# Performance work log

Measured on AMD Instinct MI355X. Metric: run time of the kernel, lower is better.

The kernel has to match this reference:

```python
import jax, jax.numpy as jnp
import numpy as np

D_MODEL, D_K, D_V, H = 1024, 64, 64, 16


def setup_inputs() -> dict:
    key = jax.random.key(0)
    ks = jax.random.split(key, 11)
    b, nq, nk = 2, 2048, 2048
    queries = jax.random.normal(ks[0], (b, nq, D_MODEL), dtype=jnp.float32)
    keys = jax.random.normal(ks[1], (b, nk, D_MODEL), dtype=jnp.float32)
    values = jax.random.normal(ks[2], (b, nk, D_MODEL), dtype=jnp.float32)
    def xavier(k, shape):
        fan_in, fan_out = shape[1], shape[0]
        lim = np.sqrt(6.0 / (fan_in + fan_out)).astype(np.float32)
        return jax.random.uniform(k, shape, jnp.float32, -lim, lim)
    # torch Linear weight shape: (out_features, in_features)
    Wq = xavier(ks[3], (H * D_K, D_MODEL)); bq = jnp.zeros((H * D_K,), jnp.float32)
    Wk = xavier(ks[4], (H * D_K, D_MODEL)); bk = jnp.zeros((H * D_K,), jnp.float32)
    Wv = xavier(ks[5], (H * D_V, D_MODEL)); bv = jnp.zeros((H * D_V,), jnp.float32)
    Wo = xavier(ks[6], (D_MODEL, H * D_V)); bo = jnp.zeros((D_MODEL,), jnp.float32)
    return {"queries": queries, "keys": keys, "values": values,
            "Wq": Wq, "bq": bq, "Wk": Wk, "bk": bk,
            "Wv": Wv, "bv": bv, "Wo": Wo, "bo": bo}


def reference(queries, keys, values, Wq, bq, Wk, bk, Wv, bv, Wo, bo):
    b, nq, _ = queries.shape
    nk = keys.shape[1]
    scale = 1.0 / np.sqrt(D_K).astype(np.float32)
    # projections -> (b, h, n, d)
    q = (queries @ Wq.T + bq).reshape(b, nq, H, D_K).transpose(0, 2, 1, 3)
    k = (keys @ Wk.T + bk).reshape(b, nk, H, D_K).transpose(0, 2, 1, 3)
    v = (values @ Wv.T + bv).reshape(b, nk, H, D_V).transpose(0, 2, 1, 3)
    att = jnp.einsum('bhqd,bhkd->bhqk', q, k) * scale  # (b,h,nq,nk)
    att = jax.nn.softmax(att, axis=-1)
    out = jnp.einsum('bhqk,bhkd->bhqd', att, v)        # (b,h,nq,dv)
    out = out.transpose(0, 2, 1, 3).reshape(b, nq, H * D_V)
    return out @ Wo.T + bo
```

## Files before the change

kernel.cpp:

```cpp
#include <hip/hip_runtime.h>
#include <stdint.h>

typedef __bf16 v8bf __attribute__((ext_vector_type(8)));
typedef float  v4f  __attribute__((ext_vector_type(4)));

#define QSCALE 0.18033688011112042f

typedef __attribute__((address_space(3))) void lds_vp;
typedef const __attribute__((address_space(1))) void gbl_vp;
__device__ __forceinline__ void gl_lds16(const __bf16* g, __bf16* l) {
    __builtin_amdgcn_global_load_lds((gbl_vp*)g, (lds_vp*)l, 16, 0, 0);
}

__device__ __forceinline__ v8bf cvt8(const float* __restrict__ p) {
    float4 x = *reinterpret_cast<const float4*>(p);
    float4 y = *reinterpret_cast<const float4*>(p + 4);
    v8bf r;
    r[0] = (__bf16)x.x; r[1] = (__bf16)x.y; r[2] = (__bf16)x.z; r[3] = (__bf16)x.w;
    r[4] = (__bf16)y.x; r[5] = (__bf16)y.y; r[6] = (__bf16)y.z; r[7] = (__bf16)y.w;
    return r;
}

__global__ __launch_bounds__(256) void cvt_w(
    const float* __restrict__ w0, const float* __restrict__ w1,
    const float* __restrict__ w2, const float* __restrict__ w3,
    __bf16* __restrict__ o0, __bf16* __restrict__ o1,
    __bf16* __restrict__ o2, __bf16* __restrict__ o3)
{
    const float* src; __bf16* dst;
    switch (blockIdx.y) {
        case 0: src = w0; dst = o0; break;
        case 1: src = w1; dst = o1; break;
        case 2: src = w2; dst = o2; break;
        default: src = w3; dst = o3; break;
    }
    size_t i = ((size_t)blockIdx.x * 256 + threadIdx.x) * 8;
    *reinterpret_cast<v8bf*>(dst + i) = cvt8(src + i);
}

__global__ __launch_bounds__(256) void cvt_in(
    const float* __restrict__ i0, const float* __restrict__ i1,
    const float* __restrict__ i2,
    __bf16* __restrict__ o0, __bf16* __restrict__ o1, __bf16* __restrict__ o2)
{
    const float* src; __bf16* dst;
    switch (blockIdx.y) {
        case 0: src = i0; dst = o0; break;
        case 1: src = i1; dst = o1; break;
        default: src = i2; dst = o2; break;
    }
    size_t i = ((size_t)blockIdx.x * 256 + threadIdx.x) * 8;
    *reinterpret_cast<v8bf*>(dst + i) = cvt8(src + i);
}

template<int MT>
__device__ __forceinline__ void gemm_body(
    const __bf16* __restrict__ A, const __bf16* __restrict__ W,
    const float* __restrict__ bias, void* __restrict__ outp,
    int mode, float oscale, int bx, int by)
{
    constexpr int K = 1024, N = 1024;
    constexpr int WM = MT / 32;
    constexpr int AI = MT / 32;
    constexpr int BI = 4;
    __shared__ __align__(16) __bf16 As[MT * 64];
    __shared__ __align__(16) __bf16 Bs[128 * 64];

    const int lane = threadIdx.x & 63;
    const int wave = threadIdx.x >> 6;
    const int quad = lane >> 4;
    const int l15  = lane & 15;
    const int m_base = bx * MT;
    const int n_base = by * 128;
    const int wm = (wave & 1) * (MT / 2);
    const int wn = (wave >> 1) * 64;

    int arow[AI], acol[AI], brow[BI], bcol[BI];
    #pragma unroll
    for (int i = 0; i < AI; ++i) {
        int L = (i * 4 + wave) * 64 + lane;
        int r = L >> 3, s = L & 7;
        arow[i] = r; acol[i] = (s ^ (r & 7)) * 8;
    }
    #pragma unroll
    for (int i = 0; i < BI; ++i) {
        int L = (i * 4 + wave) * 64 + lane;
        int r = L >> 3, s = L & 7;
        brow[i] = r; bcol[i] = (s ^ (r & 7)) * 8;
    }

    v4f acc[WM][4];
    #pragma unroll
    for (int fa = 0; fa < WM; ++fa)
        #pragma unroll
        for (int fb = 0; fb < 4; ++fb) { v4f z = {0.f,0.f,0.f,0.f}; acc[fa][fb] = z; }

    for (int kb = 0; kb < K; kb += 64) {
        #pragma unroll
        for (int i = 0; i < AI; ++i)
            gl_lds16(A + (size_t)(m_base + arow[i]) * K + kb + acol[i],
                     &As[(size_t)(i * 4 + wave) * 512]);
        #pragma unroll
        for (int i = 0; i < BI; ++i)
            gl_lds16(W + (size_t)(n_base + brow[i]) * K + kb + bcol[i],
                     &Bs[(size_t)(i * 4 + wave) * 512]);
        __syncthreads();
        #pragma unroll
        for (int ks = 0; ks < 2; ++ks) {
            v8bf af[WM], bf[4];
            #pragma unroll
            for (int f = 0; f < WM; ++f) {
                const int R = wm + f * 16 + l15;
                const int slot = (ks * 4 + quad) ^ (R & 7);
                af[f] = *reinterpret_cast<const v8bf*>(&As[R * 64 + slot * 8]);
            }
            #pragma unroll
            for (int f = 0; f < 4; ++f) {
                const int R = wn + f * 16 + l15;
                const int slot = (ks * 4 + quad) ^ (R & 7);
                bf[f] = *reinterpret_cast<const v8bf*>(&Bs[R * 64 + slot * 8]);
            }
            #pragma unroll
            for (int fa = 0; fa < WM; ++fa)
                #pragma unroll
                for (int fb = 0; fb < 4; ++fb)
                    acc[fa][fb] = __builtin_amdgcn_mfma_f32_16x16x32_bf16(
                        af[fa], bf[fb], acc[fa][fb], 0, 0, 0);
        }
        __syncthreads();
    }

    #pragma unroll
    for (int fa = 0; fa < WM; ++fa)
        #pragma unroll
        for (int fb = 0; fb < 4; ++fb) {
            const int nc = n_base + wn + fb * 16 + l15;
            const float bval = bias[nc];
            #pragma unroll
            for (int r = 0; r < 4; ++r) {
                const int m = m_base + wm + fa * 16 + quad * 4 + r;
                const float v = (acc[fa][fb][r] + bval) * oscale;
                if (mode == 2) {
                    ((float*)outp)[(size_t)m * N + nc] = v;
                } else {
                    int b = m >> 11, n = m & 2047, h = nc >> 6, d = nc & 63;
                    size_t off = (mode == 0)
                        ? ((size_t)(b * 16 + h) * 2048 + n) * 64 + d
                        : ((size_t)(b * 16 + h) * 64 + d) * 2048 + n;
                    ((__bf16*)outp)[off] = (__bf16)v;
                }
            }
        }
}

__global__ __launch_bounds__(256) void qkv_gemm(
    const __bf16* __restrict__ Aq, const __bf16* __restrict__ Ak,
    const __bf16* __restrict__ Av,
    const __bf16* __restrict__ Wq, const __bf16* __restrict__ Wk,
    const __bf16* __restrict__ Wv,
    const float* __restrict__ bq, const float* __restrict__ bk,
    const float* __restrict__ bv,
    __bf16* __restrict__ Qo, __bf16* __restrict__ Ko, __bf16* __restrict__ Vo)
{
    const int id = blockIdx.x;
    const int by = id & 7;
    const int bx = (id >> 3) & 31;
    const int z  = id >> 8;

    const __bf16 *A, *W; const float* bias; __bf16* outp; float oscale; int mode;
    switch (z) {
        case 0:  A = Aq; W = Wq; bias = bq; outp = Qo; oscale = QSCALE; mode = 0; break;
        case 1:  A = Ak; W = Wk; bias = bk; outp = Ko; oscale = 1.0f;   mode = 0; break;
        default: A = Av; W = Wv; bias = bv; outp = Vo; oscale = 1.0f;   mode = 1; break;
    }
    gemm_body<128>(A, W, bias, outp, mode, oscale, bx, by);
}

__global__ __launch_bounds__(256) void out_gemm(
    const __bf16* __restrict__ A, const __bf16* __restrict__ W,
    const float* __restrict__ bias, float* __restrict__ outp)
{
    const int by = blockIdx.x & 7;
    const int bx = blockIdx.x >> 3;
    gemm_body<64>(A, W, bias, outp, 2, 1.0f, bx, by);
}

__global__ __launch_bounds__(256) void attn_kernel(
    const __bf16* __restrict__ Q, const __bf16* __restrict__ Kb_,
    const __bf16* __restrict__ Vt, __bf16* __restrict__ O)
{
    __shared__ __align__(16) __bf16 Ks[64 * 64];
    __shared__ __align__(16) __bf16 Vs[64 * 64];
    __shared__ __align__(16) __bf16 p_lds[4][16][72];

    const int lane = threadIdx.x & 63;
    const int wave = threadIdx.x >> 6;
    const int quad = lane >> 4;
    const int l15  = lane & 15;
    const int bh = blockIdx.x & 31;
    const int qt = blockIdx.x >> 5;
    const int b  = bh >> 4, h = bh & 15;

    const __bf16* Qh = Q   + (size_t)bh * 2048 * 64;
    const __bf16* Kh = Kb_ + (size_t)bh * 2048 * 64;
    const __bf16* Vh = Vt  + (size_t)bh * 64 * 2048;

    int srow[2], scol[2];
    #pragma unroll
    for (int i = 0; i < 2; ++i) {
        int L = (i * 4 + wave) * 64 + lane;
        int r = L >> 3, s = L & 7;
        srow[i] = r; scol[i] = (s ^ (r & 7)) * 8;
    }

    v8bf qf[2];
    #pragma unroll
    for (int ks = 0; ks < 2; ++ks)
        qf[ks] = *reinterpret_cast<const v8bf*>(
            Qh + (size_t)(qt * 64 + wave * 16 + l15) * 64 + ks * 32 + quad * 8);

    v4f o_acc[4];
    #pragma unroll
    for (int c = 0; c < 4; ++c) { v4f z = {0.f,0.f,0.f,0.f}; o_acc[c] = z; }
    float l_r[4];
    #pragma unroll
    for (int r = 0; r < 4; ++r) l_r[r] = 0.f;

    for (int kt = 0; kt < 32; ++kt) {
        #pragma unroll
        for (int i = 0; i < 2; ++i) {
            gl_lds16(Kh + (size_t)(kt * 64 + srow[i]) * 64 + scol[i],
                     &Ks[(size_t)(i * 4 + wave) * 512]);
            gl_lds16(Vh + (size_t)srow[i] * 2048 + kt * 64 + scol[i],
                     &Vs[(size_t)(i * 4 + wave) * 512]);
        }
        __syncthreads();

        v4f s_t[4];
        #pragma unroll
        for (int c = 0; c < 4; ++c) { v4f z = {0.f,0.f,0.f,0.f}; s_t[c] = z; }
        #pragma unroll
        for (int ks = 0; ks < 2; ++ks) {
            v8bf kf[4];
            #pragma unroll
            for (int c = 0; c < 4; ++c) {
                const int R = c * 16 + l15;
                const int slot = (ks * 4 + quad) ^ (R & 7);
                kf[c] = *reinterpret_cast<const v8bf*>(&Ks[R * 64 + slot * 8]);
            }
            #pragma unroll
            for (int c = 0; c < 4; ++c)
                s_t[c] = __builtin_amdgcn_mfma_f32_16x16x32_bf16(qf[ks], kf[c], s_t[c], 0, 0, 0);
        }

        #pragma unroll
        for (int r = 0; r < 4; ++r) {
            const float p0 = __builtin_exp2f(s_t[0][r]);
            const float p1 = __builtin_exp2f(s_t[1][r]);
            const float p2 = __builtin_exp2f(s_t[2][r]);
            const float p3 = __builtin_exp2f(s_t[3][r]);
            l_r[r] += (p0 + p1) + (p2 + p3);
            p_lds[wave][quad * 4 + r][0 * 16 + l15] = (__bf16)p0;
            p_lds[wave][quad * 4 + r][1 * 16 + l15] = (__bf16)p1;
            p_lds[wave][quad * 4 + r][2 * 16 + l15] = (__bf16)p2;
            p_lds[wave][quad * 4 + r][3 * 16 + l15] = (__bf16)p3;
        }

        #pragma unroll
        for (int ks = 0; ks < 2; ++ks) {
            v8bf vf[4];
            #pragma unroll
            for (int c = 0; c < 4; ++c) {
                const int R = c * 16 + l15;
                const int slot = (ks * 4 + quad) ^ (R & 7);
                vf[c] = *reinterpret_cast<const v8bf*>(&Vs[R * 64 + slot * 8]);
            }
            v8bf pf = *reinterpret_cast<const v8bf*>(&p_lds[wave][l15][ks * 32 + quad * 8]);
            #pragma unroll
            for (int c = 0; c < 4; ++c)
                o_acc[c] = __builtin_amdgcn_mfma_f32_16x16x32_bf16(pf, vf[c], o_acc[c], 0, 0, 0);
        }
        __syncthreads();
    }

    #pragma unroll
    for (int r = 0; r < 4; ++r) {
        float l = l_r[r];
        #pragma unroll
        for (int off = 1; off < 16; off <<= 1)
            l += __shfl_xor(l, off, 16);
        const float inv_l = 1.0f / l;
        const int qr = qt * 64 + wave * 16 + quad * 4 + r;
        #pragma unroll
        for (int c = 0; c < 4; ++c) {
            const int col = h * 64 + c * 16 + l15;
            O[(size_t)(b * 2048 + qr) * 1024 + col] = (__bf16)(o_acc[c][r] * inv_l);
        }
    }
}

extern "C" void kernel_launch(void* const* d_in, const int* in_sizes, int n_in,
                              void* d_out, int out_size, void* d_ws, size_t ws_size,
                              hipStream_t stream) {
    const float* q_in = (const float*)d_in[0];
    const float* k_in = (const float*)d_in[1];
    const float* v_in = (const float*)d_in[2];
    const float* Wq = (const float*)d_in[3];
    const float* bq = (const float*)d_in[4];
    const float* Wk = (const float*)d_in[5];
    const float* bk = (const float*)d_in[6];
    const float* Wv = (const float*)d_in[7];
    const float* bv = (const float*)d_in[8];
    const float* Wo = (const float*)d_in[9];
    const float* bo = (const float*)d_in[10];
    float* out = (float*)d_out;

    __bf16* ws  = (__bf16*)d_ws;
    __bf16* Abq = ws;
    __bf16* Abk = Abq + 4194304;
    __bf16* Abv = Abk + 4194304;
    __bf16* Qb  = Abv + 4194304;
    __bf16* Kb  = Qb  + 4194304;
    __bf16* Vb  = Kb  + 4194304;
    __bf16* Wqb = Vb  + 4194304;
    __bf16* Wkb = Wqb + 1048576;
    __bf16* Wvb = Wkb + 1048576;
    __bf16* Wob = Wvb + 1048576;
    __bf16* Ob  = Abq;

    cvt_w<<<dim3(512, 4), 256, 0, stream>>>(Wq, Wk, Wv, Wo, Wqb, Wkb, Wvb, Wob);
    cvt_in<<<dim3(2048, 3), 256, 0, stream>>>(q_in, k_in, v_in, Abq, Abk, Abv);

    qkv_gemm<<<768, 256, 0, stream>>>(
        Abq, Abk, Abv, Wqb, Wkb, Wvb, bq, bk, bv, Qb, Kb, Vb);

    attn_kernel<<<1024, 256, 0, stream>>>(Qb, Kb, Vb, Ob);

    out_gemm<<<512, 256, 0, stream>>>(Ob, Wob, bo, out);
}
```

Measured before the change: 265.7 us.

## Prefetch next GEMM and attention tiles into registers instead of direct global-to-LDS loads

Replaces the global_load_lds direct-to-LDS copies in both the projection GEMM and the attention kernel with register-staged loads. Each iteration writes the previously fetched registers to LDS, syncs, then issues global loads for the next tile so they overlap with the MFMA compute. This hides global memory latency behind compute but adds register pressure and extra LDS write instructions. The wrap-around index makes the final iteration issue one redundant load.

```diff
diff --git a/kernel.cpp b/kernel.cpp
--- a/kernel.cpp
+++ b/kernel.cpp
@@ -5,12 +5,6 @@
 typedef float  v4f  __attribute__((ext_vector_type(4)));
 
 #define QSCALE 0.18033688011112042f
-
-typedef __attribute__((address_space(3))) void lds_vp;
-typedef const __attribute__((address_space(1))) void gbl_vp;
-__device__ __forceinline__ void gl_lds16(const __bf16* g, __bf16* l) {
-    __builtin_amdgcn_global_load_lds((gbl_vp*)g, (lds_vp*)l, 16, 0, 0);
-}
 
 __device__ __forceinline__ v8bf cvt8(const float* __restrict__ p) {
     float4 x = *reinterpret_cast<const float4*>(p);
@@ -89,6 +83,14 @@
         brow[i] = r; bcol[i] = (s ^ (r & 7)) * 8;
     }
 
+    v8bf areg[AI], wreg[BI];
+    #pragma unroll
+    for (int i = 0; i < AI; ++i)
+        areg[i] = *reinterpret_cast<const v8bf*>(A + (size_t)(m_base + arow[i]) * K + acol[i]);
+    #pragma unroll
+    for (int i = 0; i < BI; ++i)
+        wreg[i] = *reinterpret_cast<const v8bf*>(W + (size_t)(n_base + brow[i]) * K + bcol[i]);
+
     v4f acc[WM][4];
     #pragma unroll
     for (int fa = 0; fa < WM; ++fa)
@@ -98,13 +100,20 @@
     for (int kb = 0; kb < K; kb += 64) {
         #pragma unroll
         for (int i = 0; i < AI; ++i)
-            gl_lds16(A + (size_t)(m_base + arow[i]) * K + kb + acol[i],
-                     &As[(size_t)(i * 4 + wave) * 512]);
+            *reinterpret_cast<v8bf*>(&As[(i * 4 + wave) * 512 + lane * 8]) = areg[i];
         #pragma unroll
         for (int i = 0; i < BI; ++i)
-            gl_lds16(W + (size_t)(n_base + brow[i]) * K + kb + bcol[i],
-                     &Bs[(size_t)(i * 4 + wave) * 512]);
+            *reinterpret_cast<v8bf*>(&Bs[(i * 4 + wave) * 512 + lane * 8]) = wreg[i];
         __syncthreads();
+
+        const int kn = (kb + 64) & 1023;
+        #pragma unroll
+        for (int i = 0; i < AI; ++i)
+            areg[i] = *reinterpret_cast<const v8bf*>(A + (size_t)(m_base + arow[i]) * K + kn + acol[i]);
+        #pragma unroll
+        for (int i = 0; i < BI; ++i)
+            wreg[i] = *reinterpret_cast<const v8bf*>(W + (size_t)(n_base + brow[i]) * K + kn + bcol[i]);
+
         #pragma unroll
         for (int ks = 0; ks < 2; ++ks) {
             v8bf af[WM], bf[4];
@@ -219,6 +228,13 @@
         qf[ks] = *reinterpret_cast<const v8bf*>(
             Qh + (size_t)(qt * 64 + wave * 16 + l15) * 64 + ks * 32 + quad * 8);
 
+    v8bf kreg[2], vreg[2];
+    #pragma unroll
+    for (int i = 0; i < 2; ++i) {
+        kreg[i] = *reinterpret_cast<const v8bf*>(Kh + (size_t)srow[i] * 64 + scol[i]);
+        vreg[i] = *reinterpret_cast<const v8bf*>(Vh + (size_t)srow[i] * 2048 + scol[i]);
+    }
+
     v4f o_acc[4];
     #pragma unroll
     for (int c = 0; c < 4; ++c) { v4f z = {0.f,0.f,0.f,0.f}; o_acc[c] = z; }
@@ -229,12 +245,19 @@
     for (int kt = 0; kt < 32; ++kt) {
         #pragma unroll
         for (int i = 0; i < 2; ++i) {
-            gl_lds16(Kh + (size_t)(kt * 64 + srow[i]) * 64 + scol[i],
-                     &Ks[(size_t)(i * 4 + wave) * 512]);
-            gl_lds16(Vh + (size_t)srow[i] * 2048 + kt * 64 + scol[i],
-                     &Vs[(size_t)(i * 4 + wave) * 512]);
+            *reinterpret_cast<v8bf*>(&Ks[(i * 4 + wave) * 512 + lane * 8]) = kreg[i];
+            *reinterpret_cast<v8bf*>(&Vs[(i * 4 + wave) * 512 + lane * 8]) = vreg[i];
         }
         __syncthreads();
+
+        const int ktn = (kt + 1) & 31;
+        #pragma unroll
+        for (int i = 0; i < 2; ++i) {
+            kreg[i] = *reinterpret_cast<const v8bf*>(
+                Kh + (size_t)(ktn * 64 + srow[i]) * 64 + scol[i]);
+            vreg[i] = *reinterpret_cast<const v8bf*>(
+                Vh + (size_t)srow[i] * 2048 + ktn * 64 + scol[i]);
+        }
 
         v4f s_t[4];
         #pragma unroll
```

After: 260.7 us. Within noise of the previous version (-1.9%).
